# Kernel optimization log

Measured on AMD Instinct MI355X. Metric: run time of the kernel, lower is better.

The kernel has to match this reference:

```python
import jax, jax.numpy as jnp
import numpy as np

NEG_SLOPE = 0.2  # DenseGATConv default negative_slope


def _add_self_loops(adj):
    n = adj.shape[-1]
    idx = jnp.arange(n)
    return adj.at[:, idx, idx].set(1.0)


def dense_gat_conv(x, adj, W, att_src, att_dst, bias, concat):
    """PyG DenseGATConv forward (eval mode, add_loop=True).
    x: [B,N,F], adj: [B,N,N] (0/1), W: [F,H*C], att_*: [H,C], bias: [H*C] or [C]."""
    B, N, _ = x.shape
    H, C = att_src.shape
    h = (x @ W).reshape(B, N, H, C)                     # projected features
    a_src = jnp.einsum('bnhc,hc->bnh', h, att_src)      # [B,N,H]
    a_dst = jnp.einsum('bnhc,hc->bnh', h, att_dst)      # [B,N,H]
    # alpha[b,i,j,h] = a_src[b,j,h] + a_dst[b,i,h]
    alpha = a_src[:, None, :, :] + a_dst[:, :, None, :]  # [B,N,N,H]
    alpha = jax.nn.leaky_relu(alpha, NEG_SLOPE)
    adj = _add_self_loops(adj)
    alpha = jnp.where(adj[..., None] == 0, -jnp.inf, alpha)
    alpha = jax.nn.softmax(alpha, axis=2)               # softmax over sources j
    out = jnp.einsum('bijh,bjhc->bihc', alpha, h)       # [B,N,H,C]
    out = out.reshape(B, N, H * C) if concat else out.mean(axis=2)
    return out + bias


def setup_inputs() -> dict:
    key = jax.random.key(0)
    ks = jax.random.split(key, 10)
    B, N, F, H, C, NC = 1, 4096, 512, 8, 64, 16
    x = jax.random.normal(ks[0], (B, N, F), dtype=jnp.float32)
    adj = (jax.random.uniform(ks[1], (B, N, N)) < 0.01).astype(jnp.float32)
    s1 = 1.0 / np.sqrt(F)
    s2 = 1.0 / np.sqrt(H * C)
    return {
        'x': x,
        'adj': adj,
        'W1': jax.random.normal(ks[2], (F, H * C), dtype=jnp.float32) * s1,
        'att_src1': jax.random.normal(ks[3], (H, C), dtype=jnp.float32) * s1,
        'att_dst1': jax.random.normal(ks[4], (H, C), dtype=jnp.float32) * s1,
        'b1': jnp.zeros((H * C,), dtype=jnp.float32),
        'W2': jax.random.normal(ks[5], (H * C, NC), dtype=jnp.float32) * s2,
        'att_src2': jax.random.normal(ks[6], (1, NC), dtype=jnp.float32) * s2,
        'att_dst2': jax.random.normal(ks[7], (1, NC), dtype=jnp.float32) * s2,
        'b2': jnp.zeros((NC,), dtype=jnp.float32),
    }


def reference(x, adj, W1, att_src1, att_dst1, b1, W2, att_src2, att_dst2, b2):
    # eval mode: all dropout(p=0.6) layers are identity
    h = dense_gat_conv(x, adj, W1, att_src1, att_dst1, b1, concat=True)
    h = jax.nn.elu(h)
    out = dense_gat_conv(h, adj, W2, att_src2, att_dst2, b2, concat=False)
    return out
```

## Files before the change

kernel.cpp:

```cpp
#include <hip/hip_runtime.h>
#include <hip/hip_bf16.h>
#include <hip/hip_fp16.h>

#define N_NODES 4096
#define F_IN    512
#define HC      512
#define H_HEADS 8
#define C_DIM   64
#define NCLS    16
#define CAP     192
#define NEG_SLOPE 0.2f

typedef __bf16 bf16x8 __attribute__((ext_vector_type(8)));
typedef float  f32x4  __attribute__((ext_vector_type(4)));
typedef unsigned short us8 __attribute__((ext_vector_type(8)));


#define XBLKS 1024
#define WBLKS 64
#define GBLKS 512

__global__ __launch_bounds__(256) void k_split(const float* __restrict__ x,
                                               const float* __restrict__ W,
                                               ushort* __restrict__ xhi,
                                               ushort* __restrict__ xlo,
                                               ushort* __restrict__ whiT,
                                               ushort* __restrict__ wloT) {
    __shared__ float tile[64][65];
    int b = blockIdx.x;
    int t = threadIdx.x;
    if (b < XBLKS) {
        int tid = b * 256 + t;
        int rg = tid >> 10;
        int c  = tid & 1023;
        int kb = c >> 6;
        int l  = c & 63;
        int row = rg * 16 + (l & 15);
        int kbase = kb * 32 + (l >> 4) * 8;
        const float* src = &x[(size_t)row * F_IN + kbase];
        float4 v0 = *(const float4*)&src[0];
        float4 v1 = *(const float4*)&src[4];
        float f[8] = {v0.x, v0.y, v0.z, v0.w, v1.x, v1.y, v1.z, v1.w};
        us8 hv, lv;
#pragma unroll
        for (int u = 0; u < 8; ++u) {
            __bf16 h = (__bf16)f[u];
            __bf16 lo_ = (__bf16)(f[u] - (float)h);
            hv[u] = __builtin_bit_cast(unsigned short, h);
            lv[u] = __builtin_bit_cast(unsigned short, lo_);
        }
        *(us8*)&xhi[(size_t)tid * 8] = hv;
        *(us8*)&xlo[(size_t)tid * 8] = lv;
    } else {
        int bb = b - XBLKS;
        int n0 = (bb & 7) * 64, k0 = (bb >> 3) * 64;
#pragma unroll
        for (int i = 0; i < 4; ++i) {
            int r = i * 16 + (t >> 4);
            int c = (t & 15) * 4;
            *(float4*)&tile[r][c] = *(const float4*)&W[(size_t)(k0 + r) * HC + n0 + c];
        }
        __syncthreads();
        int rg_local = t >> 6;
        int l = t & 63;
        int n_local = rg_local * 16 + (l & 15);
#pragma unroll
        for (int kb_local = 0; kb_local < 2; ++kb_local) {
            int k_local = kb_local * 32 + (l >> 4) * 8;
            us8 hv, lv;
#pragma unroll
            for (int u = 0; u < 8; ++u) {
                float f = tile[k_local + u][n_local];
                __bf16 h = (__bf16)f;
                __bf16 lo_ = (__bf16)(f - (float)h);
                hv[u] = __builtin_bit_cast(unsigned short, h);
                lv[u] = __builtin_bit_cast(unsigned short, lo_);
            }
            int rg = (n0 >> 4) + rg_local;
            int kb = (k0 >> 5) + kb_local;
            size_t off = ((size_t)(rg * 16 + kb) * 64 + l) * 8;
            *(us8*)&whiT[off] = hv;
            *(us8*)&wloT[off] = lv;
        }
    }
}

__global__ __launch_bounds__(256) void k_gemm1(const ushort* __restrict__ Ahi,
                                               const ushort* __restrict__ Alo,
                                               const ushort* __restrict__ Bhi,
                                               const ushort* __restrict__ Blo,
                                               const float* __restrict__ att_src,
                                               const float* __restrict__ att_dst,
                                               const float* __restrict__ adj,
                                               __half* __restrict__ C,
                                               float* __restrict__ a_src,
                                               float* __restrict__ a_dst,
                                               int* __restrict__ row_cnt,
                                               int* __restrict__ col_idx) {
    __shared__ __align__(16) ushort smem[4][2048];
    __shared__ float s_s[2][64], s_d[2][64];
    __shared__ int cnt_s;
    int b = blockIdx.x;
    int t = threadIdx.x;
    if (b >= GBLKS) {
        int i = b - GBLKS;
        if (t == 0) cnt_s = 0;
        __syncthreads();
        const float4* row = (const float4*)(adj + (size_t)i * N_NODES);
        int* cols = col_idx + (size_t)i * CAP;
#pragma unroll
        for (int it = 0; it < 4; ++it) {
            int idx4 = it * 256 + t;
            float4 v = row[idx4];
            int j0 = idx4 * 4;
            if (v.x != 0.f && j0 + 0 != i) { int p = atomicAdd(&cnt_s, 1); if (p < CAP - 1) cols[p] = j0 + 0; }
            if (v.y != 0.f && j0 + 1 != i) { int p = atomicAdd(&cnt_s, 1); if (p < CAP - 1) cols[p] = j0 + 1; }
            if (v.z != 0.f && j0 + 2 != i) { int p = atomicAdd(&cnt_s, 1); if (p < CAP - 1) cols[p] = j0 + 2; }
            if (v.w != 0.f && j0 + 3 != i) { int p = atomicAdd(&cnt_s, 1); if (p < CAP - 1) cols[p] = j0 + 3; }
        }
        __syncthreads();
        if (t == 0) {
            int p = min(cnt_s, CAP - 1);
            cols[p] = i;
            row_cnt[i] = p + 1;
        }
        return;
    }
    int w = t >> 6, lane = t & 63;
    int head = b & 7;
    int n0 = head * 64;
    int m0 = (b >> 3) * 64;
    const ushort* src = (w == 0) ? Ahi : (w == 1) ? Alo : (w == 2) ? Bhi : Blo;
    int rg0 = ((w < 2) ? m0 : n0) >> 4;
    int mw = (w & 1) * 32, nw = (w >> 1) * 32;
    f32x4 acc[2][2] = {};
    for (int kb = 0; kb < 16; ++kb) {
#pragma unroll
        for (int g = 0; g < 4; ++g) {
            const ushort* gp = src + ((size_t)((rg0 + g) * 16 + kb) * 64 + lane) * 8;
            __builtin_amdgcn_global_load_lds(
                (const __attribute__((address_space(1))) void*)gp,
                (__attribute__((address_space(3))) void*)&smem[w][g * 512],
                16, 0, 0);
        }
        __syncthreads();
        bf16x8 ahi[2], alo[2], bhi[2], blo[2];
#pragma unroll
        for (int mi = 0; mi < 2; ++mi) {
            int g = (mw >> 4) + mi;
            ahi[mi] = __builtin_bit_cast(bf16x8, *(const us8*)&smem[0][g * 512 + lane * 8]);
            alo[mi] = __builtin_bit_cast(bf16x8, *(const us8*)&smem[1][g * 512 + lane * 8]);
        }
#pragma unroll
        for (int ni = 0; ni < 2; ++ni) {
            int g = (nw >> 4) + ni;
            bhi[ni] = __builtin_bit_cast(bf16x8, *(const us8*)&smem[2][g * 512 + lane * 8]);
            blo[ni] = __builtin_bit_cast(bf16x8, *(const us8*)&smem[3][g * 512 + lane * 8]);
        }
#pragma unroll
        for (int mi = 0; mi < 2; ++mi)
#pragma unroll
            for (int ni = 0; ni < 2; ++ni) {
                acc[mi][ni] = __builtin_amdgcn_mfma_f32_16x16x32_bf16(ahi[mi], bhi[ni], acc[mi][ni], 0, 0, 0);
                acc[mi][ni] = __builtin_amdgcn_mfma_f32_16x16x32_bf16(alo[mi], bhi[ni], acc[mi][ni], 0, 0, 0);
                acc[mi][ni] = __builtin_amdgcn_mfma_f32_16x16x32_bf16(ahi[mi], blo[ni], acc[mi][ni], 0, 0, 0);
            }
        __syncthreads();
    }
    int r0 = (lane >> 4) * 4;
    int cn = lane & 15;
    float as0 = att_src[n0 + nw + cn],      as1 = att_src[n0 + nw + 16 + cn];
    float ad0 = att_dst[n0 + nw + cn],      ad1 = att_dst[n0 + nw + 16 + cn];
#pragma unroll
    for (int mi = 0; mi < 2; ++mi)
#pragma unroll
        for (int r = 0; r < 4; ++r) {
            float ps = acc[mi][0][r] * as0 + acc[mi][1][r] * as1;
            float pd = acc[mi][0][r] * ad0 + acc[mi][1][r] * ad1;
#pragma unroll
            for (int o = 1; o < 16; o <<= 1) {
                ps += __shfl_xor(ps, o, 64);
                pd += __shfl_xor(pd, o, 64);
            }
            if (cn == 0) {
                int row = mw + mi * 16 + r0 + r;
                s_s[w >> 1][row] = ps;
                s_d[w >> 1][row] = pd;
            }
        }
#pragma unroll
    for (int mi = 0; mi < 2; ++mi)
#pragma unroll
        for (int ni = 0; ni < 2; ++ni) {
            size_t base = (size_t)(m0 + mw + mi * 16 + r0) * HC + (n0 + nw + ni * 16 + cn);
#pragma unroll
            for (int r = 0; r < 4; ++r)
                C[base + (size_t)r * HC] = __float2half(acc[mi][ni][r]);
        }
    __syncthreads();
    if (t < 64) {
        a_src[(m0 + t) * H_HEADS + head] = s_s[0][t] + s_s[1][t];
        a_dst[(m0 + t) * H_HEADS + head] = s_d[0][t] + s_d[1][t];
    }
}

__global__ __launch_bounds__(256) void k_agg1(const __half* __restrict__ hf,
                                              const float* __restrict__ a_src,
                                              const float* __restrict__ a_dst,
                                              const int* __restrict__ row_cnt,
                                              const int* __restrict__ col_idx,
                                              const float* __restrict__ b1,
                                              const float* __restrict__ W2,
                                              const float* __restrict__ att_src2,
                                              const float* __restrict__ att_dst2,
                                              float* __restrict__ h2,
                                              float* __restrict__ a_src2,
                                              float* __restrict__ a_dst2) {
    int i = blockIdx.x;
    int t = threadIdx.x;
    __shared__ float wL[CAP][H_HEADS];
    __shared__ int   colL[CAP];
    __shared__ float denom[H_HEADS];
    __shared__ float ad[H_HEADS];
    __shared__ float elu_s[HC];
    __shared__ float part[16][17];
    int cnt = row_cnt[i];
    if (t < H_HEADS) ad[t] = a_dst[i * H_HEADS + t];
    for (int j = t; j < cnt; j += 256) colL[j] = col_idx[(size_t)i * CAP + j];
    __syncthreads();
    for (int idx = t; idx < cnt * H_HEADS; idx += 256) {
        int j = idx >> 3, h = idx & 7;
        float l = a_src[colL[j] * H_HEADS + h] + ad[h];
        l = (l > 0.f) ? l : NEG_SLOPE * l;
        wL[j][h] = __expf(l);
    }
    __syncthreads();
    {
        int h = t >> 5, l32 = t & 31;
        float s = 0.f;
        for (int j = l32; j < cnt; j += 32) s += wL[j][h];
#pragma unroll
        for (int o = 16; o > 0; o >>= 1) s += __shfl_down(s, o, 32);
        if (l32 == 0) denom[h] = s;
    }
    __syncthreads();
    int e = t * 2;
    int h = e >> 6;
    float ax = 0.f, ay = 0.f;
    int j = 0;
    for (; j + 4 <= cnt; j += 4) {
        int c0 = colL[j], c1 = colL[j + 1], c2 = colL[j + 2], c3 = colL[j + 3];
        float2 v0 = __half22float2(*(const __half2*)&hf[(size_t)c0 * HC + e]);
        float2 v1 = __half22float2(*(const __half2*)&hf[(size_t)c1 * HC + e]);
        float2 v2 = __half22float2(*(const __half2*)&hf[(size_t)c2 * HC + e]);
        float2 v3 = __half22float2(*(const __half2*)&hf[(size_t)c3 * HC + e]);
        float w0 = wL[j][h], w1 = wL[j + 1][h], w2 = wL[j + 2][h], w3 = wL[j + 3][h];
        ax += w0 * v0.x + w1 * v1.x + w2 * v2.x + w3 * v3.x;
        ay += w0 * v0.y + w1 * v1.y + w2 * v2.y + w3 * v3.y;
    }
    for (; j < cnt; ++j) {
        int c0 = colL[j];
        float2 v0 = __half22float2(*(const __half2*)&hf[(size_t)c0 * HC + e]);
        float w0 = wL[j][h];
        ax += w0 * v0.x;
        ay += w0 * v0.y;
    }
    float inv = 1.f / denom[h];
    float o0 = ax * inv + b1[e];
    float o1 = ay * inv + b1[e + 1];
    o0 = (o0 > 0.f) ? o0 : (__expf(o0) - 1.f);
    o1 = (o1 > 0.f) ? o1 : (__expf(o1) - 1.f);
    elu_s[e]     = o0;
    elu_s[e + 1] = o1;
    __syncthreads();
    int kg = t >> 4, c = t & 15;
    float p = 0.f;
    const float* w2p = W2 + (size_t)kg * 32 * NCLS + c;
    const float* es  = &elu_s[kg * 32];
#pragma unroll 8
    for (int kk = 0; kk < 32; ++kk) p += es[kk] * w2p[kk * NCLS];
    part[kg][c] = p;
    __syncthreads();
    if (t < 16) {
        float s = 0.f;
#pragma unroll
        for (int r = 0; r < 16; ++r) s += part[r][t];
        h2[(size_t)i * NCLS + t] = s;
        float vs = s * att_src2[t], vd = s * att_dst2[t];
#pragma unroll
        for (int o = 8; o > 0; o >>= 1) {
            vs += __shfl_xor(vs, o, 64);
            vd += __shfl_xor(vd, o, 64);
        }
        if (t == 0) { a_src2[i] = vs; a_dst2[i] = vd; }
    }
}

__global__ __launch_bounds__(256) void k_agg2(const float* __restrict__ h2,
                                              const float* __restrict__ a_src2,
                                              const float* __restrict__ a_dst2,
                                              const int* __restrict__ row_cnt,
                                              const int* __restrict__ col_idx,
                                              const float* __restrict__ b2,
                                              float* __restrict__ out) {
    int t = threadIdx.x;
    int w = t >> 6, lane = t & 63;
    int i = blockIdx.x * 4 + w;
    __shared__ float ew[4][CAP];
    __shared__ int   colL[4][CAP];
    int cnt = row_cnt[i];
    float adi = a_dst2[i];
    float sum = 0.f;
    for (int j = lane; j < cnt; j += 64) {
        int col = col_idx[(size_t)i * CAP + j];
        colL[w][j] = col;
        float l = a_src2[col] + adi;
        l = (l > 0.f) ? l : NEG_SLOPE * l;
        float e = __expf(l);
        ew[w][j] = e;
        sum += e;
    }
#pragma unroll
    for (int o = 32; o > 0; o >>= 1) sum += __shfl_xor(sum, o, 64);
    int q = lane >> 4, c = lane & 15;
    float acc = 0.f;
    for (int j = q; j < cnt; j += 4)
        acc += ew[w][j] * h2[(size_t)colL[w][j] * NCLS + c];
    acc += __shfl_down(acc, 32, 64);
    acc += __shfl_down(acc, 16, 64);
    if (lane < NCLS)
        out[(size_t)i * NCLS + lane] = acc / sum + b2[lane];
}

extern "C" void kernel_launch(void* const* d_in, const int* in_sizes, int n_in,
                              void* d_out, int out_size, void* d_ws, size_t ws_size,
                              hipStream_t stream) {
    const float* x        = (const float*)d_in[0];
    const float* adj      = (const float*)d_in[1];
    const float* W1       = (const float*)d_in[2];
    const float* att_src1 = (const float*)d_in[3];
    const float* att_dst1 = (const float*)d_in[4];
    const float* b1       = (const float*)d_in[5];
    const float* W2       = (const float*)d_in[6];
    const float* att_src2 = (const float*)d_in[7];
    const float* att_dst2 = (const float*)d_in[8];
    const float* b2       = (const float*)d_in[9];
    float* out = (float*)d_out;

    char* ws = (char*)d_ws;
    int*    row_cnt = (int*)ws;     ws += (size_t)N_NODES * 4;
    int*    col_idx = (int*)ws;     ws += (size_t)N_NODES * CAP * 4;
    __half* h1f     = (__half*)ws;  ws += (size_t)N_NODES * HC * 2;
    float*  a_src   = (float*)ws;   ws += (size_t)N_NODES * H_HEADS * 4;
    float*  a_dst   = (float*)ws;   ws += (size_t)N_NODES * H_HEADS * 4;
    float*  h2      = (float*)ws;   ws += (size_t)N_NODES * NCLS * 4;
    float*  as2     = (float*)ws;   ws += (size_t)N_NODES * 4;
    float*  ad2     = (float*)ws;   ws += (size_t)N_NODES * 4;
    ushort* x_hi    = (ushort*)ws;  ws += (size_t)N_NODES * F_IN * 2;
    ushort* x_lo    = (ushort*)ws;  ws += (size_t)N_NODES * F_IN * 2;
    ushort* w_hiT   = (ushort*)ws;  ws += (size_t)F_IN * HC * 2;
    ushort* w_loT   = (ushort*)ws;  ws += (size_t)F_IN * HC * 2;

    hipLaunchKernelGGL(k_split, dim3(XBLKS + WBLKS), dim3(256), 0, stream,
                       x, W1, x_hi, x_lo, w_hiT, w_loT);
    hipLaunchKernelGGL(k_gemm1, dim3(GBLKS + N_NODES), dim3(256), 0, stream,
                       x_hi, x_lo, w_hiT, w_loT, att_src1, att_dst1, adj,
                       h1f, a_src, a_dst, row_cnt, col_idx);
    hipLaunchKernelGGL(k_agg1, dim3(N_NODES), dim3(256), 0, stream,
                       h1f, a_src, a_dst, row_cnt, col_idx, b1,
                       W2, att_src2, att_dst2, h2, as2, ad2);
    hipLaunchKernelGGL(k_agg2, dim3(N_NODES / 4), dim3(256), 0, stream,
                       h2, as2, ad2, row_cnt, col_idx, b2, out);
}
```

Measured before the change: 154.6 us.

## Fuse bf16 hi/lo split into GEMM1 loads and widen aggregation unroll

Removes the separate split kernel and its workspace round trip. GEMM1 now reads fp32 x and W1 directly and converts each tile to bf16 hi/lo pairs in registers before storing to shared memory. The block-to-tile mapping is swapped so consecutive blocks share the same W1 head, and the aggregation gather loop is unrolled by 8. The cost is redundant conversion work in every GEMM block, strided scalar W1 loads in place of async global-to-LDS copies, and higher register pressure.

```diff
diff --git a/kernel.cpp b/kernel.cpp
--- a/kernel.cpp
+++ b/kernel.cpp
@@ -15,80 +15,11 @@
 typedef float  f32x4  __attribute__((ext_vector_type(4)));
 typedef unsigned short us8 __attribute__((ext_vector_type(8)));
 
-
-#define XBLKS 1024
-#define WBLKS 64
 #define GBLKS 512
 
-__global__ __launch_bounds__(256) void k_split(const float* __restrict__ x,
-                                               const float* __restrict__ W,
-                                               ushort* __restrict__ xhi,
-                                               ushort* __restrict__ xlo,
-                                               ushort* __restrict__ whiT,
-                                               ushort* __restrict__ wloT) {
-    __shared__ float tile[64][65];
-    int b = blockIdx.x;
-    int t = threadIdx.x;
-    if (b < XBLKS) {
-        int tid = b * 256 + t;
-        int rg = tid >> 10;
-        int c  = tid & 1023;
-        int kb = c >> 6;
-        int l  = c & 63;
-        int row = rg * 16 + (l & 15);
-        int kbase = kb * 32 + (l >> 4) * 8;
-        const float* src = &x[(size_t)row * F_IN + kbase];
-        float4 v0 = *(const float4*)&src[0];
-        float4 v1 = *(const float4*)&src[4];
-        float f[8] = {v0.x, v0.y, v0.z, v0.w, v1.x, v1.y, v1.z, v1.w};
-        us8 hv, lv;
-#pragma unroll
-        for (int u = 0; u < 8; ++u) {
-            __bf16 h = (__bf16)f[u];
-            __bf16 lo_ = (__bf16)(f[u] - (float)h);
-            hv[u] = __builtin_bit_cast(unsigned short, h);
-            lv[u] = __builtin_bit_cast(unsigned short, lo_);
-        }
-        *(us8*)&xhi[(size_t)tid * 8] = hv;
-        *(us8*)&xlo[(size_t)tid * 8] = lv;
-    } else {
-        int bb = b - XBLKS;
-        int n0 = (bb & 7) * 64, k0 = (bb >> 3) * 64;
-#pragma unroll
-        for (int i = 0; i < 4; ++i) {
-            int r = i * 16 + (t >> 4);
-            int c = (t & 15) * 4;
-            *(float4*)&tile[r][c] = *(const float4*)&W[(size_t)(k0 + r) * HC + n0 + c];
-        }
-        __syncthreads();
-        int rg_local = t >> 6;
-        int l = t & 63;
-        int n_local = rg_local * 16 + (l & 15);
-#pragma unroll
-        for (int kb_local = 0; kb_local < 2; ++kb_local) {
-            int k_local = kb_local * 32 + (l >> 4) * 8;
-            us8 hv, lv;
-#pragma unroll
-            for (int u = 0; u < 8; ++u) {
-                float f = tile[k_local + u][n_local];
-                __bf16 h = (__bf16)f;
-                __bf16 lo_ = (__bf16)(f - (float)h);
-                hv[u] = __builtin_bit_cast(unsigned short, h);
-                lv[u] = __builtin_bit_cast(unsigned short, lo_);
-            }
-            int rg = (n0 >> 4) + rg_local;
-            int kb = (k0 >> 5) + kb_local;
-            size_t off = ((size_t)(rg * 16 + kb) * 64 + l) * 8;
-            *(us8*)&whiT[off] = hv;
-            *(us8*)&wloT[off] = lv;
-        }
-    }
-}
-
-__global__ __launch_bounds__(256) void k_gemm1(const ushort* __restrict__ Ahi,
-                                               const ushort* __restrict__ Alo,
-                                               const ushort* __restrict__ Bhi,
-                                               const ushort* __restrict__ Blo,
+
+__global__ __launch_bounds__(256) void k_gemm1(const float* __restrict__ x,
+                                               const float* __restrict__ W1,
                                                const float* __restrict__ att_src,
                                                const float* __restrict__ att_dst,
                                                const float* __restrict__ adj,
@@ -97,7 +28,7 @@
                                                float* __restrict__ a_dst,
                                                int* __restrict__ row_cnt,
                                                int* __restrict__ col_idx) {
-    __shared__ __align__(16) ushort smem[4][2048];
+    __shared__ __align__(16) ushort sAhi[2048], sAlo[2048], sBhi[2048], sBlo[2048];
     __shared__ float s_s[2][64], s_d[2][64];
     __shared__ int cnt_s;
     int b = blockIdx.x;
@@ -127,35 +58,55 @@
         return;
     }
     int w = t >> 6, lane = t & 63;
-    int head = b & 7;
+    int head = b >> 6;
     int n0 = head * 64;
-    int m0 = (b >> 3) * 64;
-    const ushort* src = (w == 0) ? Ahi : (w == 1) ? Alo : (w == 2) ? Bhi : Blo;
-    int rg0 = ((w < 2) ? m0 : n0) >> 4;
+    int m0 = (b & 63) * 64;
     int mw = (w & 1) * 32, nw = (w >> 1) * 32;
+    int g0 = (w & 1) * 2;
+    bool isB = (w >> 1) != 0;
     f32x4 acc[2][2] = {};
     for (int kb = 0; kb < 16; ++kb) {
 #pragma unroll
-        for (int g = 0; g < 4; ++g) {
-            const ushort* gp = src + ((size_t)((rg0 + g) * 16 + kb) * 64 + lane) * 8;
-            __builtin_amdgcn_global_load_lds(
-                (const __attribute__((address_space(1))) void*)gp,
-                (__attribute__((address_space(3))) void*)&smem[w][g * 512],
-                16, 0, 0);
+        for (int gg = 0; gg < 2; ++gg) {
+            int g  = g0 + gg;
+            int rn = (isB ? n0 : m0) + g * 16 + (lane & 15);
+            int kk = kb * 32 + (lane >> 4) * 8;
+            float f[8];
+            if (!isB) {
+                float4 v0 = *(const float4*)&x[(size_t)rn * F_IN + kk];
+                float4 v1 = *(const float4*)&x[(size_t)rn * F_IN + kk + 4];
+                f[0] = v0.x; f[1] = v0.y; f[2] = v0.z; f[3] = v0.w;
+                f[4] = v1.x; f[5] = v1.y; f[6] = v1.z; f[7] = v1.w;
+            } else {
+#pragma unroll
+                for (int u = 0; u < 8; ++u) f[u] = W1[(size_t)(kk + u) * HC + rn];
+            }
+            us8 hv, lv;
+#pragma unroll
+            for (int u = 0; u < 8; ++u) {
+                __bf16 h = (__bf16)f[u];
+                __bf16 lo_ = (__bf16)(f[u] - (float)h);
+                hv[u] = __builtin_bit_cast(unsigned short, h);
+                lv[u] = __builtin_bit_cast(unsigned short, lo_);
+            }
+            ushort* dh = isB ? sBhi : sAhi;
+            ushort* dl = isB ? sBlo : sAlo;
+            *(us8*)&dh[g * 512 + lane * 8] = hv;
+            *(us8*)&dl[g * 512 + lane * 8] = lv;
         }
         __syncthreads();
         bf16x8 ahi[2], alo[2], bhi[2], blo[2];
 #pragma unroll
         for (int mi = 0; mi < 2; ++mi) {
             int g = (mw >> 4) + mi;
-            ahi[mi] = __builtin_bit_cast(bf16x8, *(const us8*)&smem[0][g * 512 + lane * 8]);
-            alo[mi] = __builtin_bit_cast(bf16x8, *(const us8*)&smem[1][g * 512 + lane * 8]);
+            ahi[mi] = __builtin_bit_cast(bf16x8, *(const us8*)&sAhi[g * 512 + lane * 8]);
+            alo[mi] = __builtin_bit_cast(bf16x8, *(const us8*)&sAlo[g * 512 + lane * 8]);
         }
 #pragma unroll
         for (int ni = 0; ni < 2; ++ni) {
             int g = (nw >> 4) + ni;
-            bhi[ni] = __builtin_bit_cast(bf16x8, *(const us8*)&smem[2][g * 512 + lane * 8]);
-            blo[ni] = __builtin_bit_cast(bf16x8, *(const us8*)&smem[3][g * 512 + lane * 8]);
+            bhi[ni] = __builtin_bit_cast(bf16x8, *(const us8*)&sBhi[g * 512 + lane * 8]);
+            blo[ni] = __builtin_bit_cast(bf16x8, *(const us8*)&sBlo[g * 512 + lane * 8]);
         }
 #pragma unroll
         for (int mi = 0; mi < 2; ++mi)
@@ -248,6 +199,24 @@
     int h = e >> 6;
     float ax = 0.f, ay = 0.f;
     int j = 0;
+    for (; j + 8 <= cnt; j += 8) {
+        int c0 = colL[j],     c1 = colL[j + 1], c2 = colL[j + 2], c3 = colL[j + 3];
+        int c4 = colL[j + 4], c5 = colL[j + 5], c6 = colL[j + 6], c7 = colL[j + 7];
+        float2 v0 = __half22float2(*(const __half2*)&hf[(size_t)c0 * HC + e]);
+        float2 v1 = __half22float2(*(const __half2*)&hf[(size_t)c1 * HC + e]);
+        float2 v2 = __half22float2(*(const __half2*)&hf[(size_t)c2 * HC + e]);
+        float2 v3 = __half22float2(*(const __half2*)&hf[(size_t)c3 * HC + e]);
+        float2 v4 = __half22float2(*(const __half2*)&hf[(size_t)c4 * HC + e]);
+        float2 v5 = __half22float2(*(const __half2*)&hf[(size_t)c5 * HC + e]);
+        float2 v6 = __half22float2(*(const __half2*)&hf[(size_t)c6 * HC + e]);
+        float2 v7 = __half22float2(*(const __half2*)&hf[(size_t)c7 * HC + e]);
+        float w0 = wL[j][h],     w1 = wL[j + 1][h], w2 = wL[j + 2][h], w3 = wL[j + 3][h];
+        float w4 = wL[j + 4][h], w5 = wL[j + 5][h], w6 = wL[j + 6][h], w7 = wL[j + 7][h];
+        ax += w0 * v0.x + w1 * v1.x + w2 * v2.x + w3 * v3.x
+            + w4 * v4.x + w5 * v5.x + w6 * v6.x + w7 * v7.x;
+        ay += w0 * v0.y + w1 * v1.y + w2 * v2.y + w3 * v3.y
+            + w4 * v4.y + w5 * v5.y + w6 * v6.y + w7 * v7.y;
+    }
     for (; j + 4 <= cnt; j += 4) {
         int c0 = colL[j], c1 = colL[j + 1], c2 = colL[j + 2], c3 = colL[j + 3];
         float2 v0 = __half22float2(*(const __half2*)&hf[(size_t)c0 * HC + e]);
@@ -356,15 +325,9 @@
     float*  h2      = (float*)ws;   ws += (size_t)N_NODES * NCLS * 4;
     float*  as2     = (float*)ws;   ws += (size_t)N_NODES * 4;
     float*  ad2     = (float*)ws;   ws += (size_t)N_NODES * 4;
-    ushort* x_hi    = (ushort*)ws;  ws += (size_t)N_NODES * F_IN * 2;
-    ushort* x_lo    = (ushort*)ws;  ws += (size_t)N_NODES * F_IN * 2;
-    ushort* w_hiT   = (ushort*)ws;  ws += (size_t)F_IN * HC * 2;
-    ushort* w_loT   = (ushort*)ws;  ws += (size_t)F_IN * HC * 2;
-
-    hipLaunchKernelGGL(k_split, dim3(XBLKS + WBLKS), dim3(256), 0, stream,
-                       x, W1, x_hi, x_lo, w_hiT, w_loT);
+
     hipLaunchKernelGGL(k_gemm1, dim3(GBLKS + N_NODES), dim3(256), 0, stream,
-                       x_hi, x_lo, w_hiT, w_loT, att_src1, att_dst1, adj,
+                       x, W1, att_src1, att_dst1, adj,
                        h1f, a_src, a_dst, row_cnt, col_idx);
     hipLaunchKernelGGL(k_agg1, dim3(N_NODES), dim3(256), 0, stream,
                        h1f, a_src, a_dst, row_cnt, col_idx, b1,
```

Result: slower. 160.6 us (+3.8%).

## Process two nodes per agg1 block with wider half loads, remap gemm tile order

Applied to the files above, without the earlier changes.

The layer-1 aggregation kernel now handles two destination nodes per 256-thread block, 128 threads each. Each thread accumulates four features using 8-byte half loads with an 8-way unrolled neighbor loop, and the W2 projection is split into 8 groups of 64. Separately, the GEMM block index mapping is changed so consecutive blocks walk along row tiles within a head rather than across heads, which changes L2 reuse of the A/B tiles. Halving the block count raises per-thread work and memory-level parallelism but doubles shared-memory use per block.

```diff
diff --git a/kernel.cpp b/kernel.cpp
--- a/kernel.cpp
+++ b/kernel.cpp
@@ -127,9 +127,9 @@
         return;
     }
     int w = t >> 6, lane = t & 63;
-    int head = b & 7;
+    int head = b >> 6;
     int n0 = head * 64;
-    int m0 = (b >> 3) * 64;
+    int m0 = (b & 63) * 64;
     const ushort* src = (w == 0) ? Ahi : (w == 1) ? Alo : (w == 2) ? Bhi : Blo;
     int rg0 = ((w < 2) ? m0 : n0) >> 4;
     int mw = (w & 1) * 32, nw = (w >> 1) * 32;
@@ -216,83 +216,97 @@
                                               float* __restrict__ h2,
                                               float* __restrict__ a_src2,
                                               float* __restrict__ a_dst2) {
-    int i = blockIdx.x;
     int t = threadIdx.x;
-    __shared__ float wL[CAP][H_HEADS];
-    __shared__ int   colL[CAP];
-    __shared__ float denom[H_HEADS];
-    __shared__ float ad[H_HEADS];
-    __shared__ float elu_s[HC];
-    __shared__ float part[16][17];
+    int r = t >> 7;
+    int tt = t & 127;
+    int i = blockIdx.x * 2 + r;
+    __shared__ float wL[2][CAP][H_HEADS];
+    __shared__ int   colL[2][CAP];
+    __shared__ float denom[2][H_HEADS];
+    __shared__ float ad[2][H_HEADS];
+    __shared__ float elu_s[2][HC];
+    __shared__ float part[2][8][17];
     int cnt = row_cnt[i];
-    if (t < H_HEADS) ad[t] = a_dst[i * H_HEADS + t];
-    for (int j = t; j < cnt; j += 256) colL[j] = col_idx[(size_t)i * CAP + j];
-    __syncthreads();
-    for (int idx = t; idx < cnt * H_HEADS; idx += 256) {
+    if (tt < H_HEADS) ad[r][tt] = a_dst[i * H_HEADS + tt];
+    for (int j = tt; j < cnt; j += 128) colL[r][j] = col_idx[(size_t)i * CAP + j];
+    __syncthreads();
+    for (int idx = tt; idx < cnt * H_HEADS; idx += 128) {
         int j = idx >> 3, h = idx & 7;
-        float l = a_src[colL[j] * H_HEADS + h] + ad[h];
+        float l = a_src[colL[r][j] * H_HEADS + h] + ad[r][h];
         l = (l > 0.f) ? l : NEG_SLOPE * l;
-        wL[j][h] = __expf(l);
+        wL[r][j][h] = __expf(l);
     }
     __syncthreads();
     {
-        int h = t >> 5, l32 = t & 31;
+        int h = tt >> 4, l16 = tt & 15;
         float s = 0.f;
-        for (int j = l32; j < cnt; j += 32) s += wL[j][h];
-#pragma unroll
-        for (int o = 16; o > 0; o >>= 1) s += __shfl_down(s, o, 32);
-        if (l32 == 0) denom[h] = s;
-    }
-    __syncthreads();
-    int e = t * 2;
-    int h = e >> 6;
-    float ax = 0.f, ay = 0.f;
+        for (int j = l16; j < cnt; j += 16) s += wL[r][j][h];
+#pragma unroll
+        for (int o = 8; o > 0; o >>= 1) s += __shfl_down(s, o, 16);
+        if (l16 == 0) denom[r][h] = s;
+    }
+    __syncthreads();
+    int e = tt * 4;
+    int h = tt >> 4;
+    float a0 = 0.f, a1 = 0.f, a2 = 0.f, a3 = 0.f;
     int j = 0;
-    for (; j + 4 <= cnt; j += 4) {
-        int c0 = colL[j], c1 = colL[j + 1], c2 = colL[j + 2], c3 = colL[j + 3];
-        float2 v0 = __half22float2(*(const __half2*)&hf[(size_t)c0 * HC + e]);
-        float2 v1 = __half22float2(*(const __half2*)&hf[(size_t)c1 * HC + e]);
-        float2 v2 = __half22float2(*(const __half2*)&hf[(size_t)c2 * HC + e]);
-        float2 v3 = __half22float2(*(const __half2*)&hf[(size_t)c3 * HC + e]);
-        float w0 = wL[j][h], w1 = wL[j + 1][h], w2 = wL[j + 2][h], w3 = wL[j + 3][h];
-        ax += w0 * v0.x + w1 * v1.x + w2 * v2.x + w3 * v3.x;
-        ay += w0 * v0.y + w1 * v1.y + w2 * v2.y + w3 * v3.y;
+    for (; j + 8 <= cnt; j += 8) {
+#pragma unroll
+        for (int u = 0; u < 8; ++u) {
+            int c = colL[r][j + u];
+            uint2 q = *(const uint2*)&hf[(size_t)c * HC + e];
+            float2 f01 = __half22float2(__builtin_bit_cast(__half2, q.x));
+            float2 f23 = __half22float2(__builtin_bit_cast(__half2, q.y));
+            float wj = wL[r][j + u][h];
+            a0 += wj * f01.x; a1 += wj * f01.y;
+            a2 += wj * f23.x; a3 += wj * f23.y;
+        }
     }
     for (; j < cnt; ++j) {
-        int c0 = colL[j];
-        float2 v0 = __half22float2(*(const __half2*)&hf[(size_t)c0 * HC + e]);
-        float w0 = wL[j][h];
-        ax += w0 * v0.x;
-        ay += w0 * v0.y;
-    }
-    float inv = 1.f / denom[h];
-    float o0 = ax * inv + b1[e];
-    float o1 = ay * inv + b1[e + 1];
+        int c = colL[r][j];
+        uint2 q = *(const uint2*)&hf[(size_t)c * HC + e];
+        float2 f01 = __half22float2(__builtin_bit_cast(__half2, q.x));
+        float2 f23 = __half22float2(__builtin_bit_cast(__half2, q.y));
+        float wj = wL[r][j][h];
+        a0 += wj * f01.x; a1 += wj * f01.y;
+        a2 += wj * f23.x; a3 += wj * f23.y;
+    }
+    float inv = 1.f / denom[r][h];
+    float o0 = a0 * inv + b1[e];
+    float o1 = a1 * inv + b1[e + 1];
+    float o2 = a2 * inv + b1[e + 2];
+    float o3 = a3 * inv + b1[e + 3];
     o0 = (o0 > 0.f) ? o0 : (__expf(o0) - 1.f);
     o1 = (o1 > 0.f) ? o1 : (__expf(o1) - 1.f);
-    elu_s[e]     = o0;
-    elu_s[e + 1] = o1;
-    __syncthreads();
-    int kg = t >> 4, c = t & 15;
-    float p = 0.f;
-    const float* w2p = W2 + (size_t)kg * 32 * NCLS + c;
-    const float* es  = &elu_s[kg * 32];
+    o2 = (o2 > 0.f) ? o2 : (__expf(o2) - 1.f);
+    o3 = (o3 > 0.f) ? o3 : (__expf(o3) - 1.f);
+    elu_s[r][e]     = o0;
+    elu_s[r][e + 1] = o1;
+    elu_s[r][e + 2] = o2;
+    elu_s[r][e + 3] = o3;
+    __syncthreads();
+    {
+        int kg = tt >> 4, c = tt & 15;
+        float p = 0.f;
+        const float* w2p = W2 + (size_t)kg * 64 * NCLS + c;
+        const float* es  = &elu_s[r][kg * 64];
 #pragma unroll 8
-    for (int kk = 0; kk < 32; ++kk) p += es[kk] * w2p[kk * NCLS];
-    part[kg][c] = p;
-    __syncthreads();
-    if (t < 16) {
+        for (int kk = 0; kk < 64; ++kk) p += es[kk] * w2p[kk * NCLS];
+        part[r][kg][c] = p;
+    }
+    __syncthreads();
+    if (tt < 16) {
         float s = 0.f;
 #pragma unroll
-        for (int r = 0; r < 16; ++r) s += part[r][t];
-        h2[(size_t)i * NCLS + t] = s;
-        float vs = s * att_src2[t], vd = s * att_dst2[t];
+        for (int g = 0; g < 8; ++g) s += part[r][g][tt];
+        h2[(size_t)i * NCLS + tt] = s;
+        float vs = s * att_src2[tt], vd = s * att_dst2[tt];
 #pragma unroll
         for (int o = 8; o > 0; o >>= 1) {
-            vs += __shfl_xor(vs, o, 64);
-            vd += __shfl_xor(vd, o, 64);
-        }
-        if (t == 0) { a_src2[i] = vs; a_dst2[i] = vd; }
+            vs += __shfl_xor(vs, o, 16);
+            vd += __shfl_xor(vd, o, 16);
+        }
+        if (tt == 0) { a_src2[i] = vs; a_dst2[i] = vd; }
     }
 }
 
@@ -366,7 +380,7 @@
     hipLaunchKernelGGL(k_gemm1, dim3(GBLKS + N_NODES), dim3(256), 0, stream,
                        x_hi, x_lo, w_hiT, w_loT, att_src1, att_dst1, adj,
                        h1f, a_src, a_dst, row_cnt, col_idx);
-    hipLaunchKernelGGL(k_agg1, dim3(N_NODES), dim3(256), 0, stream,
+    hipLaunchKernelGGL(k_agg1, dim3(N_NODES / 2), dim3(256), 0, stream,
                        h1f, a_src, a_dst, row_cnt, col_idx, b1,
                        W2, att_src2, att_dst2, h2, as2, ad2);
     hipLaunchKernelGGL(k_agg2, dim3(N_NODES / 4), dim3(256), 0, stream,
```

Measured after the change: 149.9 us. 3.1% less time.
